# Performance work log

Measured on AMD Instinct MI355X. Metric: run time of the kernel, lower is better.

The kernel has to match this reference:

```python
import jax, jax.numpy as jnp
import numpy as np

TEMPERATURE = 1.0
MAX_ITERS = 10
EPSILON = 1e-4
N, D, K = 131072, 64, 64


def setup_inputs() -> dict:
    key = jax.random.key(0)
    k1, k2 = jax.random.split(key)
    weights = jax.random.normal(k1, (N, D), dtype=jnp.float32)
    init_clusters = jax.random.normal(k2, (K, D), dtype=jnp.float32)
    return {"weights": weights, "init_clusters": init_clusters}


def _dkm(weights, init_clusters):
    n, d = weights.shape
    k = init_clusters.shape[0]
    w_sq = jnp.sum(weights * weights, axis=1, keepdims=True)  # [N,1]

    def step(carry, _):
        clusters, attn_prev, done = carry
        # Euclidean cdist via the expansion ||w||^2 + ||c||^2 - 2 w.c
        c_sq = jnp.sum(clusters * clusters, axis=1)               # [K]
        d2 = w_sq + c_sq[None, :] - 2.0 * (weights @ clusters.T)  # [N,K]
        dist = jnp.sqrt(jnp.maximum(d2, 0.0))
        attn = jax.nn.softmax(-dist / TEMPERATURE, axis=-1)        # [N,K]
        new_clusters = (attn.T @ weights) / jnp.sum(attn, axis=0)[:, None]  # [K,D]
        converged = jnp.linalg.norm(clusters - new_clusters) <= EPSILON
        # Torch breaks BEFORE assigning new_clusters; emulate with a done flag.
        clusters_next = jnp.where(done | converged, clusters, new_clusters)
        attn_next = jnp.where(done, attn_prev, attn)
        return (clusters_next, attn_next, done | converged), None

    init = (init_clusters, jnp.zeros((n, k), weights.dtype), jnp.array(False))
    (clusters, attn, _), _ = jax.lax.scan(step, init, None, length=MAX_ITERS)
    compressed = attn @ clusters  # [N,D]
    return compressed, clusters, attn


def reference(weights, init_clusters):
    return _dkm(weights, init_clusters)
```

## Files before the change

kernel.cpp:

```cpp
#include <hip/hip_runtime.h>
#include <math.h>
#include <stdint.h>

#define N_ROWS 131072
#define DIM 64
#define KC 64
#define NBLK 512
#define ROWS_PB 256

typedef __attribute__((ext_vector_type(8))) short short8;
typedef __attribute__((ext_vector_type(8))) unsigned short ushort8;
typedef __attribute__((ext_vector_type(16))) float float16;
typedef __attribute__((ext_vector_type(4))) unsigned int uint4v;
typedef __attribute__((ext_vector_type(2))) unsigned long long ulong2v;

#define PARTIAL_OFF 0u
#define SUMA_OFF    2097152u
#define NEWC_OFF    2129920u
#define NORM_BYTE_OFF (2134016ull * 4ull)

__device__ __forceinline__ uint32_t rne16(float a) {
  uint32_t u = __float_as_uint(a);
  return (u + 0x7fffu + ((u >> 16) & 1u)) >> 16;
}

__device__ __forceinline__ uint32_t pack_bf16(float a, float b) {
  return rne16(a) | (rne16(b) << 16);
}

__device__ __forceinline__ void split2(float a, float b, uint32_t& hi, uint32_t& lo) {
  uint32_t ha = rne16(a), hb = rne16(b);
  hi = ha | (hb << 16);
  float la = a - __uint_as_float(ha << 16);
  float lb = b - __uint_as_float(hb << 16);
  lo = pack_bf16(la, lb);
}

__global__ __launch_bounds__(256, 3) void dkm_iter(
    const float* __restrict__ W, const float* __restrict__ Cinit,
    const float* __restrict__ newC, float* __restrict__ cur,
    const double* __restrict__ normpart,
    float* __restrict__ partial, float* __restrict__ sumA,
    float* __restrict__ attn_out, int useSel, int writeAttn)
{
  __shared__ __align__(16) short CbfHi[64][68];
  __shared__ __align__(16) short CbfLo[64][68];
  __shared__ __align__(16) short attnT[64][136];
  __shared__ __align__(16) short WTsh[64][136];
  __shared__ float csqL[64];
  __shared__ float wsqL[128];
  __shared__ int s_cond;

  const int t = threadIdx.x;
  const int blk = blockIdx.x;
  const int wid = t >> 6, lane = t & 63, l31 = lane & 31, lh = lane >> 5;
  const int mg = wid >> 1, ng = wid & 1;
  const int rowBase = blk * ROWS_PB;
  const int colA = wid * 32 + l31;

  const float* pwBase = W + (size_t)(rowBase + wid * 32 + l31) * 64 + lh * 8;
  float4 vv[8];
#pragma unroll
  for (int q = 0; q < 8; ++q)
    vv[q] = *(const float4*)(pwBase + (q >> 1) * 16 + (q & 1) * 4);

  if (wid == 0) {
    double v = 0.0;
    if (useSel) {
#pragma unroll
      for (int i = 0; i < 8; ++i) v += normpart[lane + 64 * i];
    }
    v += __shfl_xor(v, 1); v += __shfl_xor(v, 2); v += __shfl_xor(v, 4);
    v += __shfl_xor(v, 8); v += __shfl_xor(v, 16); v += __shfl_xor(v, 32);
    if (lane == 0) s_cond = (v > 1.0e-8) ? 1 : 0;
  }
  __syncthreads();

  const float* src = useSel ? (s_cond ? newC : cur) : Cinit;

  {
    const int crow = t >> 2, cc = (t & 3) * 16;
    float sq = 0.f;
#pragma unroll
    for (int q = 0; q < 4; ++q) {
      float4 c0 = *(const float4*)(src + crow * 64 + cc + q * 4);
      if (blk == 0) *(float4*)(cur + crow * 64 + cc + q * 4) = c0;
      uint32_t h0, h1, l0, l1;
      split2(c0.x, c0.y, h0, l0);
      split2(c0.z, c0.w, h1, l1);
      uint32_t* ph = (uint32_t*)&CbfHi[crow][cc + q * 4];
      ph[0] = h0; ph[1] = h1;
      uint32_t* pl = (uint32_t*)&CbfLo[crow][cc + q * 4];
      pl[0] = l0; pl[1] = l1;
      sq += c0.x*c0.x + c0.y*c0.y + c0.z*c0.z + c0.w*c0.w;
    }
    sq += __shfl_xor(sq, 1);
    sq += __shfl_xor(sq, 2);
    if ((t & 3) == 0) csqL[crow] = sq;
  }
  __syncthreads();

  float16 Uacc = {0,0,0,0, 0,0,0,0, 0,0,0,0, 0,0,0,0};
  float ssumAll = 0.f;
  const float cq0 = csqL[l31], cq1 = csqL[32 + l31];

#pragma unroll
  for (int c = 0; c < 2; ++c) {
    const int chunkBase = rowBase + c * 128;

    float16 dot0 = {0,0,0,0, 0,0,0,0, 0,0,0,0, 0,0,0,0};
    float16 dot1 = {0,0,0,0, 0,0,0,0, 0,0,0,0, 0,0,0,0};
    float w2acc = 0.f;
#pragma unroll
    for (int ko = 0; ko < 4; ++ko) {
      float4 a = vv[ko * 2];
      float4 b = vv[ko * 2 + 1];
      w2acc += a.x*a.x + a.y*a.y + a.z*a.z + a.w*a.w
             + b.x*b.x + b.y*b.y + b.z*b.z + b.w*b.w;
      uint32_t h0, h1, h2, h3, l0, l1, l2, l3;
      split2(a.x, a.y, h0, l0); split2(a.z, a.w, h1, l1);
      split2(b.x, b.y, h2, l2); split2(b.z, b.w, h3, l3);
      const int d0 = ko * 16 + lh * 8;
      WTsh[d0 + 0][colA] = (short)h0;  WTsh[d0 + 1][colA] = (short)(h0 >> 16);
      WTsh[d0 + 2][colA] = (short)h1;  WTsh[d0 + 3][colA] = (short)(h1 >> 16);
      WTsh[d0 + 4][colA] = (short)h2;  WTsh[d0 + 5][colA] = (short)(h2 >> 16);
      WTsh[d0 + 6][colA] = (short)h3;  WTsh[d0 + 7][colA] = (short)(h3 >> 16);
      uint4v th = {h0, h1, h2, h3};
      uint4v tl = {l0, l1, l2, l3};
      short8 aHi = __builtin_bit_cast(short8, th);
      short8 aLo = __builtin_bit_cast(short8, tl);
#pragma unroll
      for (int nt = 0; nt < 2; ++nt) {
        const unsigned long long* ph = (const unsigned long long*)&CbfHi[nt * 32 + l31][ko * 16 + lh * 8];
        const unsigned long long* pl = (const unsigned long long*)&CbfLo[nt * 32 + l31][ko * 16 + lh * 8];
        ulong2v vh = {ph[0], ph[1]};
        ulong2v vl = {pl[0], pl[1]};
        short8 cHi = __builtin_bit_cast(short8, vh);
        short8 cLo = __builtin_bit_cast(short8, vl);
        float16& dd = nt ? dot1 : dot0;
        dd = __builtin_amdgcn_mfma_f32_32x32x16_bf16(aHi, cHi, dd, 0, 0, 0);
        dd = __builtin_amdgcn_mfma_f32_32x32x16_bf16(aLo, cHi, dd, 0, 0, 0);
        dd = __builtin_amdgcn_mfma_f32_32x32x16_bf16(aHi, cLo, dd, 0, 0, 0);
      }
    }
    w2acc += __shfl_xor(w2acc, 32);
    if (lane < 32) wsqL[wid * 32 + l31] = w2acc;

    if (c == 0) {
      const float* pwN = pwBase + 128 * 64;
#pragma unroll
      for (int q = 0; q < 8; ++q)
        vv[q] = *(const float4*)(pwN + (q >> 1) * 16 + (q & 1) * 4);
    }

#pragma unroll
    for (int j = 0; j < 16; ++j) {
      const int trow = (j & 3) + 8 * (j >> 2) + 4 * lh;
      const float w2 = wsqL[wid * 32 + trow];
      float g0 = -sqrtf(fmaxf(fmaf(-2.f, dot0[j], w2 + cq0), 0.f));
      float g1 = -sqrtf(fmaxf(fmaf(-2.f, dot1[j], w2 + cq1), 0.f));
      dot0[j] = __expf(g0);
      dot1[j] = __expf(g1);
    }

    if (writeAttn) {
#pragma unroll
      for (int j = 0; j < 16; ++j) {
        const int trow = (j & 3) + 8 * (j >> 2) + 4 * lh;
        float sj = dot0[j] + dot1[j];
        sj += __shfl_xor(sj, 1);  sj += __shfl_xor(sj, 2);  sj += __shfl_xor(sj, 4);
        sj += __shfl_xor(sj, 8);  sj += __shfl_xor(sj, 16);
        float inv = __builtin_amdgcn_rcpf(sj);
        attn_out[(size_t)(chunkBase + wid * 32 + trow) * 64 + l31] = dot0[j] * inv;
        attn_out[(size_t)(chunkBase + wid * 32 + trow) * 64 + 32 + l31] = dot1[j] * inv;
      }
    }

    {
      uint32_t* aT = (uint32_t*)&attnT[0][0];
      const int cb = wid * 16;
#pragma unroll
      for (int h = 0; h < 4; ++h) {
        const int base = cb + 4 * h + 2 * lh;
        aT[l31 * 68 + base]     = pack_bf16(dot0[4 * h],     dot0[4 * h + 1]);
        aT[l31 * 68 + base + 1] = pack_bf16(dot0[4 * h + 2], dot0[4 * h + 3]);
        aT[(32 + l31) * 68 + base]     = pack_bf16(dot1[4 * h],     dot1[4 * h + 1]);
        aT[(32 + l31) * 68 + base + 1] = pack_bf16(dot1[4 * h + 2], dot1[4 * h + 3]);
      }
    }
    __syncthreads();

    float* invsL = wsqL;
    {
      const int r = t >> 1, kh = t & 1;
      float s = 0.f;
#pragma unroll
      for (int kk = 0; kk < 32; ++kk) {
        uint32_t v = (uint32_t)(unsigned short)attnT[kh * 32 + kk][r];
        s += __uint_as_float(v << 16);
      }
      s += __shfl_xor(s, 1);
      if (kh == 0) invsL[r] = __builtin_amdgcn_rcpf(s);
    }
    __syncthreads();

    {
      const int k = t >> 2, q = t & 3;
      uint32_t* row = (uint32_t*)&attnT[k][0];
#pragma unroll
      for (int i = 0; i < 16; ++i) {
        const int ii = (i + k) & 15;
        const int r2 = q * 32 + 2 * ii;
        uint32_t dv = row[q * 16 + ii];
        float lo = __uint_as_float(dv << 16) * invsL[r2];
        float hi = __uint_as_float(dv & 0xffff0000u) * invsL[r2 + 1];
        row[q * 16 + ii] = pack_bf16(lo, hi);
      }
    }
    __syncthreads();

#pragma unroll
    for (int kc = 0; kc < 8; ++kc) {
      const unsigned long long* pa =
          (const unsigned long long*)&attnT[mg * 32 + l31][kc * 16 + lh * 8];
      ulong2v va = {pa[0], pa[1]};
      short8 af = __builtin_bit_cast(short8, va);
      const unsigned long long* pb =
          (const unsigned long long*)&WTsh[ng * 32 + l31][kc * 16 + lh * 8];
      ulong2v vb = {pb[0], pb[1]};
      short8 bf = __builtin_bit_cast(short8, vb);
      Uacc = __builtin_amdgcn_mfma_f32_32x32x16_bf16(af, bf, Uacc, 0, 0, 0);
    }

    {
      const int sk = t & 63, sg = t >> 6;
#pragma unroll
      for (int q2 = 0; q2 < 4; ++q2) {
        const uint32_t* pq = (const uint32_t*)&attnT[sk][sg * 32 + q2 * 8];
#pragma unroll
        for (int w = 0; w < 4; ++w) {
          uint32_t dv = pq[w];
          ssumAll += __uint_as_float(dv << 16) + __uint_as_float(dv & 0xffff0000u);
        }
      }
    }
    __syncthreads();
  }

#pragma unroll
  for (int j = 0; j < 16; ++j) {
    const int k = mg * 32 + (j & 3) + 8 * (j >> 2) + 4 * lh;
    partial[((size_t)blk * 64 + k) * 64 + ng * 32 + l31] = Uacc[j];
  }

  float* red = (float*)&CbfHi[0][0];
  red[t] = ssumAll;
  __syncthreads();
  if (t < 64) sumA[blk * 64 + t] = (red[t] + red[t + 64]) + (red[t + 128] + red[t + 192]);
}

__global__ __launch_bounds__(256) void reduce_kernel(
    const float* __restrict__ partial, const float* __restrict__ sumAp,
    const float* __restrict__ curC, float* __restrict__ newC,
    double* __restrict__ normpart) {
  const int k = blockIdx.x >> 3, oct = blockIdx.x & 7;
  const int t = threadIdx.x;
  const int d = oct * 8 + (t & 7), q = t >> 3;
  double acc = 0.0;
  for (int b = q * 16; b < q * 16 + 16; ++b)
    acc += (double)partial[((size_t)b * 64 + k) * 64 + d];
  __shared__ double sh[256];
  __shared__ double sh2[256];
  sh[t] = acc;
  sh2[t] = (double)sumAp[t * 64 + k] + (double)sumAp[(t + 256) * 64 + k];
  __syncthreads();
#pragma unroll
  for (int s = 128; s >= 8; s >>= 1) {
    if (t < s) { sh[t] += sh[t + s]; sh2[t] += sh2[t + s]; }
    __syncthreads();
  }
#pragma unroll
  for (int s = 4; s >= 1; s >>= 1) {
    if (t < s) sh2[t] += sh2[t + s];
    __syncthreads();
  }
  if (t < 8) {
    float nc = (float)(sh[t] / sh2[0]);
    newC[k * 64 + d] = nc;
    double diff = (double)curC[k * 64 + d] - (double)nc;
    sh[t] = diff * diff;
  }
  __syncthreads();
  if (t == 0) {
    double s = 0.0;
#pragma unroll
    for (int i = 0; i < 8; ++i) s += sh[i];
    normpart[blockIdx.x] = s;
  }
}

__global__ __launch_bounds__(256) void finalize_kernel(
    const double* __restrict__ np, const float* __restrict__ newC,
    const float* __restrict__ cur, float* __restrict__ clusters_out) {
  __shared__ double sh[64];
  __shared__ int sc;
  int t = threadIdx.x;
  if (t < 64) {
    double v = 0.0;
#pragma unroll
    for (int i = 0; i < 8; ++i) v += np[t + 64 * i];
    sh[t] = v;
  }
  __syncthreads();
  if (t == 0) {
    double s = 0.0;
    for (int i = 0; i < 64; ++i) s += sh[i];
    sc = (s > 1.0e-8) ? 1 : 0;
  }
  __syncthreads();
  const float* src = sc ? newC : cur;
  for (int m = t; m < 4096; m += 256) {
    float v = src[m];
    clusters_out[m] = v;
  }
}

__global__ __launch_bounds__(256) void compress_kernel(
    const float* __restrict__ attn, const float* __restrict__ Cl,
    float* __restrict__ outC) {
  __shared__ float Csh[64 * 64];
  __shared__ float Ash[64 * 64];
  float4* Csh4 = (float4*)Csh;
  float4* Ash4 = (float4*)Ash;
  const int t = threadIdx.x;
  const int blk = blockIdx.x;
  const int rowBase = blk * 256;
  const int rg = t >> 4, dg = t & 15;

  {
    const float4* gC = (const float4*)Cl;
#pragma unroll
    for (int q = 0; q < 4; ++q) {
      int m = t + 256 * q;
      Csh4[m ^ ((m >> 6) & 15)] = gC[m];
    }
  }

  for (int tile = 0; tile < 4; ++tile) {
    __syncthreads();
    {
      const float4* gA = (const float4*)(attn + (size_t)(rowBase + tile * 64) * KC);
#pragma unroll
      for (int q = 0; q < 4; ++q) {
        int m = t + 256 * q;
        Ash4[m ^ ((m >> 6) & 15)] = gA[m];
      }
    }
    __syncthreads();
    float acc[4][4] = {{0.f}};
#pragma unroll 4
    for (int c = 0; c < 16; ++c) {
      float4 av[4], cv[4];
#pragma unroll
      for (int i = 0; i < 4; ++i) av[i] = Ash4[((rg * 4 + i) * 16 + c) ^ rg];
#pragma unroll
      for (int j = 0; j < 4; ++j) cv[j] = Csh4[((c * 4 + j) * 16 + dg) ^ c];
#pragma unroll
      for (int i = 0; i < 4; ++i) {
        float a0 = fmaf(av[i].x, cv[0].x, acc[i][0]);
        a0 = fmaf(av[i].y, cv[1].x, a0);
        a0 = fmaf(av[i].z, cv[2].x, a0);
        acc[i][0] = fmaf(av[i].w, cv[3].x, a0);
        float a1 = fmaf(av[i].x, cv[0].y, acc[i][1]);
        a1 = fmaf(av[i].y, cv[1].y, a1);
        a1 = fmaf(av[i].z, cv[2].y, a1);
        acc[i][1] = fmaf(av[i].w, cv[3].y, a1);
        float a2 = fmaf(av[i].x, cv[0].z, acc[i][2]);
        a2 = fmaf(av[i].y, cv[1].z, a2);
        a2 = fmaf(av[i].z, cv[2].z, a2);
        acc[i][2] = fmaf(av[i].w, cv[3].z, a2);
        float a3 = fmaf(av[i].x, cv[0].w, acc[i][3]);
        a3 = fmaf(av[i].y, cv[1].w, a3);
        a3 = fmaf(av[i].z, cv[2].w, a3);
        acc[i][3] = fmaf(av[i].w, cv[3].w, a3);
      }
    }
    float4* gO = (float4*)(outC + (size_t)(rowBase + tile * 64) * DIM);
#pragma unroll
    for (int i = 0; i < 4; ++i)
      gO[(rg * 4 + i) * 16 + dg] = make_float4(acc[i][0], acc[i][1], acc[i][2], acc[i][3]);
  }
}

extern "C" void kernel_launch(void* const* d_in, const int* in_sizes, int n_in,
                              void* d_out, int out_size, void* d_ws, size_t ws_size,
                              hipStream_t stream) {
  (void)in_sizes; (void)n_in; (void)d_ws; (void)ws_size; (void)out_size;
  const float* W = (const float*)d_in[0];
  const float* Cinit = (const float*)d_in[1];
  float* ob = (float*)d_out;

  float* compressed = ob;
  float* clusters_out = ob + (size_t)N_ROWS * DIM;
  float* attn_out = ob + (size_t)N_ROWS * DIM + KC * DIM;

  float* partial = ob + PARTIAL_OFF;
  float* sumAp = ob + SUMA_OFF;
  float* newC = ob + NEWC_OFF;
  float* cur = clusters_out;
  double* normpart = (double*)((char*)d_out + NORM_BYTE_OFF);

  for (int it = 0; it < 10; ++it) {
    dkm_iter<<<NBLK, 256, 0, stream>>>(W, Cinit, newC, cur, normpart,
                                       partial, sumAp, attn_out,
                                       (it > 0) ? 1 : 0, (it == 9) ? 1 : 0);
    reduce_kernel<<<512, 256, 0, stream>>>(partial, sumAp, cur, newC, normpart);
  }
  finalize_kernel<<<1, 256, 0, stream>>>(normpart, newC, cur, clusters_out);
  compress_kernel<<<512, 256, 0, stream>>>(attn_out, clusters_out, compressed);
}
```

Baseline: 354.8 us.

## Precompute transposed bf16 weights once and compute attention column sums via MFMA

Adds a prep kernel that converts W to bf16 and writes it transposed into scratch space at the start of the output buffer. The per-iteration kernel then reads the B operand for the attn^T·W MFMA straight from global memory instead of building a transposed shared-memory tile. This frees LDS, so launch bounds now allow 4 blocks per CU. The per-cluster attention sums are computed by an extra MFMA against a vector of ones, replacing the LDS scan and reduction. In exchange, each of the 10 iterations does extra global reads of the transposed copy, and workspace offsets move, which relies on later kernels overwriting that scratch region.

```diff
diff --git a/kernel.cpp b/kernel.cpp
--- a/kernel.cpp
+++ b/kernel.cpp
@@ -14,10 +14,10 @@
 typedef __attribute__((ext_vector_type(4))) unsigned int uint4v;
 typedef __attribute__((ext_vector_type(2))) unsigned long long ulong2v;
 
-#define PARTIAL_OFF 0u
-#define SUMA_OFF    2097152u
-#define NEWC_OFF    2129920u
-#define NORM_BYTE_OFF (2134016ull * 4ull)
+#define PARTIAL_OFF 4194304u
+#define SUMA_OFF    6291456u
+#define NEWC_OFF    6324224u
+#define NORM_BYTE_OFF (6328320ull * 4ull)
 
 __device__ __forceinline__ uint32_t rne16(float a) {
   uint32_t u = __float_as_uint(a);
@@ -36,8 +36,34 @@
   lo = pack_bf16(la, lb);
 }
 
-__global__ __launch_bounds__(256, 3) void dkm_iter(
-    const float* __restrict__ W, const float* __restrict__ Cinit,
+__global__ __launch_bounds__(256) void prep_kernel(const float* __restrict__ W,
+                                                   unsigned short* __restrict__ WT) {
+  __shared__ unsigned short Tsh[64][256];
+  const int t = threadIdx.x;
+  const int blk = blockIdx.x;
+  const int r = blk * 256 + t;
+  const float4* p = (const float4*)(W + (size_t)r * DIM);
+#pragma unroll
+  for (int c = 0; c < 16; ++c) {
+    float4 v = p[c];
+    Tsh[c * 4 + 0][t] = (unsigned short)rne16(v.x);
+    Tsh[c * 4 + 1][t] = (unsigned short)rne16(v.y);
+    Tsh[c * 4 + 2][t] = (unsigned short)rne16(v.z);
+    Tsh[c * 4 + 3][t] = (unsigned short)rne16(v.w);
+  }
+  __syncthreads();
+#pragma unroll
+  for (int it = 0; it < 8; ++it) {
+    const int idx = it * 256 + t;
+    const int d = idx >> 5, c8 = (idx & 31) * 8;
+    ushort8 v = *(const ushort8*)&Tsh[d][c8];
+    *(ushort8*)(WT + (size_t)d * N_ROWS + blk * 256 + c8) = v;
+  }
+}
+
+__global__ __launch_bounds__(256, 4) void dkm_iter(
+    const float* __restrict__ W, const unsigned short* __restrict__ WT,
+    const float* __restrict__ Cinit,
     const float* __restrict__ newC, float* __restrict__ cur,
     const double* __restrict__ normpart,
     float* __restrict__ partial, float* __restrict__ sumA,
@@ -46,7 +72,6 @@
   __shared__ __align__(16) short CbfHi[64][68];
   __shared__ __align__(16) short CbfLo[64][68];
   __shared__ __align__(16) short attnT[64][136];
-  __shared__ __align__(16) short WTsh[64][136];
   __shared__ float csqL[64];
   __shared__ float wsqL[128];
   __shared__ int s_cond;
@@ -56,7 +81,6 @@
   const int wid = t >> 6, lane = t & 63, l31 = lane & 31, lh = lane >> 5;
   const int mg = wid >> 1, ng = wid & 1;
   const int rowBase = blk * ROWS_PB;
-  const int colA = wid * 32 + l31;
 
   const float* pwBase = W + (size_t)(rowBase + wid * 32 + l31) * 64 + lh * 8;
   float4 vv[8];
@@ -101,7 +125,9 @@
   __syncthreads();
 
   float16 Uacc = {0,0,0,0, 0,0,0,0, 0,0,0,0, 0,0,0,0};
-  float ssumAll = 0.f;
+  float16 Uacc1 = {0,0,0,0, 0,0,0,0, 0,0,0,0, 0,0,0,0};
+  const short8 ones = {0x3F80, 0x3F80, 0x3F80, 0x3F80,
+                       0x3F80, 0x3F80, 0x3F80, 0x3F80};
   const float cq0 = csqL[l31], cq1 = csqL[32 + l31];
 
 #pragma unroll
@@ -120,11 +146,6 @@
       uint32_t h0, h1, h2, h3, l0, l1, l2, l3;
       split2(a.x, a.y, h0, l0); split2(a.z, a.w, h1, l1);
       split2(b.x, b.y, h2, l2); split2(b.z, b.w, h3, l3);
-      const int d0 = ko * 16 + lh * 8;
-      WTsh[d0 + 0][colA] = (short)h0;  WTsh[d0 + 1][colA] = (short)(h0 >> 16);
-      WTsh[d0 + 2][colA] = (short)h1;  WTsh[d0 + 3][colA] = (short)(h1 >> 16);
-      WTsh[d0 + 4][colA] = (short)h2;  WTsh[d0 + 5][colA] = (short)(h2 >> 16);
-      WTsh[d0 + 6][colA] = (short)h3;  WTsh[d0 + 7][colA] = (short)(h3 >> 16);
       uint4v th = {h0, h1, h2, h3};
       uint4v tl = {l0, l1, l2, l3};
       short8 aHi = __builtin_bit_cast(short8, th);
@@ -219,30 +240,18 @@
     }
     __syncthreads();
 
+    const unsigned short* pwt =
+        WT + (size_t)(ng * 32 + l31) * N_ROWS + chunkBase + lh * 8;
 #pragma unroll
     for (int kc = 0; kc < 8; ++kc) {
       const unsigned long long* pa =
           (const unsigned long long*)&attnT[mg * 32 + l31][kc * 16 + lh * 8];
       ulong2v va = {pa[0], pa[1]};
       short8 af = __builtin_bit_cast(short8, va);
-      const unsigned long long* pb =
-          (const unsigned long long*)&WTsh[ng * 32 + l31][kc * 16 + lh * 8];
-      ulong2v vb = {pb[0], pb[1]};
-      short8 bf = __builtin_bit_cast(short8, vb);
+      ushort8 wv = *(const ushort8*)(pwt + kc * 16);
+      short8 bf = __builtin_bit_cast(short8, wv);
       Uacc = __builtin_amdgcn_mfma_f32_32x32x16_bf16(af, bf, Uacc, 0, 0, 0);
-    }
-
-    {
-      const int sk = t & 63, sg = t >> 6;
-#pragma unroll
-      for (int q2 = 0; q2 < 4; ++q2) {
-        const uint32_t* pq = (const uint32_t*)&attnT[sk][sg * 32 + q2 * 8];
-#pragma unroll
-        for (int w = 0; w < 4; ++w) {
-          uint32_t dv = pq[w];
-          ssumAll += __uint_as_float(dv << 16) + __uint_as_float(dv & 0xffff0000u);
-        }
-      }
+      Uacc1 = __builtin_amdgcn_mfma_f32_32x32x16_bf16(af, ones, Uacc1, 0, 0, 0);
     }
     __syncthreads();
   }
@@ -252,11 +261,13 @@
     const int k = mg * 32 + (j & 3) + 8 * (j >> 2) + 4 * lh;
     partial[((size_t)blk * 64 + k) * 64 + ng * 32 + l31] = Uacc[j];
   }
-
-  float* red = (float*)&CbfHi[0][0];
-  red[t] = ssumAll;
-  __syncthreads();
-  if (t < 64) sumA[blk * 64 + t] = (red[t] + red[t + 64]) + (red[t + 128] + red[t + 192]);
+  if (ng == 0 && l31 == 0) {
+#pragma unroll
+    for (int j = 0; j < 16; ++j) {
+      const int k = mg * 32 + (j & 3) + 8 * (j >> 2) + 4 * lh;
+      sumA[blk * 64 + k] = Uacc1[j];
+    }
+  }
 }
 
 __global__ __launch_bounds__(256) void reduce_kernel(
@@ -404,14 +415,17 @@
   float* clusters_out = ob + (size_t)N_ROWS * DIM;
   float* attn_out = ob + (size_t)N_ROWS * DIM + KC * DIM;
 
+  unsigned short* WT = (unsigned short*)d_out;
   float* partial = ob + PARTIAL_OFF;
   float* sumAp = ob + SUMA_OFF;
   float* newC = ob + NEWC_OFF;
   float* cur = clusters_out;
   double* normpart = (double*)((char*)d_out + NORM_BYTE_OFF);
 
+  prep_kernel<<<NBLK, 256, 0, stream>>>(W, WT);
+
   for (int it = 0; it < 10; ++it) {
-    dkm_iter<<<NBLK, 256, 0, stream>>>(W, Cinit, newC, cur, normpart,
+    dkm_iter<<<NBLK, 256, 0, stream>>>(W, WT, Cinit, newC, cur, normpart,
                                        partial, sumAp, attn_out,
                                        (it > 0) ? 1 : 0, (it == 9) ? 1 : 0);
     reduce_kernel<<<512, 256, 0, stream>>>(partial, sumAp, cur, newC, normpart);
```

New measurement: 416.3 us. 1.17x slower.

## Precompute bf16 hi/lo split of weights once and sum attention via MFMA

Applied to the files above, without the earlier changes.

Adds a prep kernel that splits the weights into bf16 hi/lo halves and computes the row squared norms once. The results go into the attn output buffer as scratch, so the ten iterations skip the per-iteration conversion and norm work. Bytes loaded per iteration stay the same (two bf16 halves equal one fp32). The per-cluster attention sums are now computed with an extra MFMA against a ones vector, which replaces the LDS scalar reduction loop and its final barrier. The risk is that the last iteration writes attn into the same buffer the weight split lives in, while other blocks may still be reading it.

```diff
diff --git a/kernel.cpp b/kernel.cpp
--- a/kernel.cpp
+++ b/kernel.cpp
@@ -11,13 +11,13 @@
 typedef __attribute__((ext_vector_type(8))) short short8;
 typedef __attribute__((ext_vector_type(8))) unsigned short ushort8;
 typedef __attribute__((ext_vector_type(16))) float float16;
-typedef __attribute__((ext_vector_type(4))) unsigned int uint4v;
 typedef __attribute__((ext_vector_type(2))) unsigned long long ulong2v;
 
 #define PARTIAL_OFF 0u
 #define SUMA_OFF    2097152u
-#define NEWC_OFF    2129920u
-#define NORM_BYTE_OFF (2134016ull * 4ull)
+#define WSQ_OFF     2129920u
+#define NEWC_OFF    2260992u
+#define NORM_BYTE_OFF (2265088ull * 4ull)
 
 __device__ __forceinline__ uint32_t rne16(float a) {
   uint32_t u = __float_as_uint(a);
@@ -36,12 +36,35 @@
   lo = pack_bf16(la, lb);
 }
 
+__global__ __launch_bounds__(256) void prep_kernel(const float* __restrict__ W,
+                                                   unsigned short* WS,
+                                                   float* __restrict__ wsq) {
+  const int t = threadIdx.x;
+  const int r = blockIdx.x * 256 + t;
+  const float4* p = (const float4*)(W + (size_t)r * DIM);
+  uint32_t* hi = (uint32_t*)(WS + (size_t)r * 128);
+  uint32_t* lo = hi + 32;
+  float s = 0.f;
+#pragma unroll
+  for (int c = 0; c < 16; ++c) {
+    float4 v = p[c];
+    s += v.x * v.x + v.y * v.y + v.z * v.z + v.w * v.w;
+    uint32_t h0, h1, l0, l1;
+    split2(v.x, v.y, h0, l0);
+    split2(v.z, v.w, h1, l1);
+    hi[c * 2] = h0; hi[c * 2 + 1] = h1;
+    lo[c * 2] = l0; lo[c * 2 + 1] = l1;
+  }
+  wsq[r] = s;
+}
+
 __global__ __launch_bounds__(256, 3) void dkm_iter(
-    const float* __restrict__ W, const float* __restrict__ Cinit,
+    const unsigned short* WS, const float* __restrict__ wsq,
+    const float* __restrict__ Cinit,
     const float* __restrict__ newC, float* __restrict__ cur,
     const double* __restrict__ normpart,
     float* __restrict__ partial, float* __restrict__ sumA,
-    float* __restrict__ attn_out, int useSel, int writeAttn)
+    float* attn_out, int useSel, int writeAttn)
 {
   __shared__ __align__(16) short CbfHi[64][68];
   __shared__ __align__(16) short CbfLo[64][68];
@@ -58,11 +81,14 @@
   const int rowBase = blk * ROWS_PB;
   const int colA = wid * 32 + l31;
 
-  const float* pwBase = W + (size_t)(rowBase + wid * 32 + l31) * 64 + lh * 8;
-  float4 vv[8];
-#pragma unroll
-  for (int q = 0; q < 8; ++q)
-    vv[q] = *(const float4*)(pwBase + (q >> 1) * 16 + (q & 1) * 4);
+  const unsigned short* pws =
+      WS + (size_t)(rowBase + wid * 32 + l31) * 128 + lh * 8;
+  ushort8 vh[4], vl[4];
+#pragma unroll
+  for (int ko = 0; ko < 4; ++ko) {
+    vh[ko] = *(const ushort8*)(pws + ko * 16);
+    vl[ko] = *(const ushort8*)(pws + 64 + ko * 16);
+  }
 
   if (wid == 0) {
     double v = 0.0;
@@ -101,56 +127,50 @@
   __syncthreads();
 
   float16 Uacc = {0,0,0,0, 0,0,0,0, 0,0,0,0, 0,0,0,0};
-  float ssumAll = 0.f;
+  float16 Uacc1 = {0,0,0,0, 0,0,0,0, 0,0,0,0, 0,0,0,0};
+  const short8 ones = {0x3F80, 0x3F80, 0x3F80, 0x3F80,
+                       0x3F80, 0x3F80, 0x3F80, 0x3F80};
   const float cq0 = csqL[l31], cq1 = csqL[32 + l31];
 
 #pragma unroll
   for (int c = 0; c < 2; ++c) {
     const int chunkBase = rowBase + c * 128;
 
+    if (t < 128) wsqL[t] = wsq[chunkBase + t];
+
     float16 dot0 = {0,0,0,0, 0,0,0,0, 0,0,0,0, 0,0,0,0};
     float16 dot1 = {0,0,0,0, 0,0,0,0, 0,0,0,0, 0,0,0,0};
-    float w2acc = 0.f;
 #pragma unroll
     for (int ko = 0; ko < 4; ++ko) {
-      float4 a = vv[ko * 2];
-      float4 b = vv[ko * 2 + 1];
-      w2acc += a.x*a.x + a.y*a.y + a.z*a.z + a.w*a.w
-             + b.x*b.x + b.y*b.y + b.z*b.z + b.w*b.w;
-      uint32_t h0, h1, h2, h3, l0, l1, l2, l3;
-      split2(a.x, a.y, h0, l0); split2(a.z, a.w, h1, l1);
-      split2(b.x, b.y, h2, l2); split2(b.z, b.w, h3, l3);
       const int d0 = ko * 16 + lh * 8;
-      WTsh[d0 + 0][colA] = (short)h0;  WTsh[d0 + 1][colA] = (short)(h0 >> 16);
-      WTsh[d0 + 2][colA] = (short)h1;  WTsh[d0 + 3][colA] = (short)(h1 >> 16);
-      WTsh[d0 + 4][colA] = (short)h2;  WTsh[d0 + 5][colA] = (short)(h2 >> 16);
-      WTsh[d0 + 6][colA] = (short)h3;  WTsh[d0 + 7][colA] = (short)(h3 >> 16);
-      uint4v th = {h0, h1, h2, h3};
-      uint4v tl = {l0, l1, l2, l3};
-      short8 aHi = __builtin_bit_cast(short8, th);
-      short8 aLo = __builtin_bit_cast(short8, tl);
+      WTsh[d0 + 0][colA] = vh[ko][0];  WTsh[d0 + 1][colA] = vh[ko][1];
+      WTsh[d0 + 2][colA] = vh[ko][2];  WTsh[d0 + 3][colA] = vh[ko][3];
+      WTsh[d0 + 4][colA] = vh[ko][4];  WTsh[d0 + 5][colA] = vh[ko][5];
+      WTsh[d0 + 6][colA] = vh[ko][6];  WTsh[d0 + 7][colA] = vh[ko][7];
+      short8 aHi = __builtin_bit_cast(short8, vh[ko]);
+      short8 aLo = __builtin_bit_cast(short8, vl[ko]);
 #pragma unroll
       for (int nt = 0; nt < 2; ++nt) {
         const unsigned long long* ph = (const unsigned long long*)&CbfHi[nt * 32 + l31][ko * 16 + lh * 8];
         const unsigned long long* pl = (const unsigned long long*)&CbfLo[nt * 32 + l31][ko * 16 + lh * 8];
-        ulong2v vh = {ph[0], ph[1]};
-        ulong2v vl = {pl[0], pl[1]};
-        short8 cHi = __builtin_bit_cast(short8, vh);
-        short8 cLo = __builtin_bit_cast(short8, vl);
+        ulong2v vhh = {ph[0], ph[1]};
+        ulong2v vll = {pl[0], pl[1]};
+        short8 cHi = __builtin_bit_cast(short8, vhh);
+        short8 cLo = __builtin_bit_cast(short8, vll);
         float16& dd = nt ? dot1 : dot0;
         dd = __builtin_amdgcn_mfma_f32_32x32x16_bf16(aHi, cHi, dd, 0, 0, 0);
         dd = __builtin_amdgcn_mfma_f32_32x32x16_bf16(aLo, cHi, dd, 0, 0, 0);
         dd = __builtin_amdgcn_mfma_f32_32x32x16_bf16(aHi, cLo, dd, 0, 0, 0);
       }
     }
-    w2acc += __shfl_xor(w2acc, 32);
-    if (lane < 32) wsqL[wid * 32 + l31] = w2acc;
 
     if (c == 0) {
-      const float* pwN = pwBase + 128 * 64;
-#pragma unroll
-      for (int q = 0; q < 8; ++q)
-        vv[q] = *(const float4*)(pwN + (q >> 1) * 16 + (q & 1) * 4);
+      const unsigned short* pwN = pws + 128 * 128;
+#pragma unroll
+      for (int ko = 0; ko < 4; ++ko) {
+        vh[ko] = *(const ushort8*)(pwN + ko * 16);
+        vl[ko] = *(const ushort8*)(pwN + 64 + ko * 16);
+      }
     }
 
 #pragma unroll
@@ -230,19 +250,7 @@
       ulong2v vb = {pb[0], pb[1]};
       short8 bf = __builtin_bit_cast(short8, vb);
       Uacc = __builtin_amdgcn_mfma_f32_32x32x16_bf16(af, bf, Uacc, 0, 0, 0);
-    }
-
-    {
-      const int sk = t & 63, sg = t >> 6;
-#pragma unroll
-      for (int q2 = 0; q2 < 4; ++q2) {
-        const uint32_t* pq = (const uint32_t*)&attnT[sk][sg * 32 + q2 * 8];
-#pragma unroll
-        for (int w = 0; w < 4; ++w) {
-          uint32_t dv = pq[w];
-          ssumAll += __uint_as_float(dv << 16) + __uint_as_float(dv & 0xffff0000u);
-        }
-      }
+      Uacc1 = __builtin_amdgcn_mfma_f32_32x32x16_bf16(af, ones, Uacc1, 0, 0, 0);
     }
     __syncthreads();
   }
@@ -252,11 +260,13 @@
     const int k = mg * 32 + (j & 3) + 8 * (j >> 2) + 4 * lh;
     partial[((size_t)blk * 64 + k) * 64 + ng * 32 + l31] = Uacc[j];
   }
-
-  float* red = (float*)&CbfHi[0][0];
-  red[t] = ssumAll;
-  __syncthreads();
-  if (t < 64) sumA[blk * 64 + t] = (red[t] + red[t + 64]) + (red[t + 128] + red[t + 192]);
+  if (ng == 0 && l31 == 0) {
+#pragma unroll
+    for (int j = 0; j < 16; ++j) {
+      const int k = mg * 32 + (j & 3) + 8 * (j >> 2) + 4 * lh;
+      sumA[blk * 64 + k] = Uacc1[j];
+    }
+  }
 }
 
 __global__ __launch_bounds__(256) void reduce_kernel(
@@ -404,14 +414,18 @@
   float* clusters_out = ob + (size_t)N_ROWS * DIM;
   float* attn_out = ob + (size_t)N_ROWS * DIM + KC * DIM;
 
+  unsigned short* WS = (unsigned short*)attn_out;
   float* partial = ob + PARTIAL_OFF;
   float* sumAp = ob + SUMA_OFF;
+  float* wsq = ob + WSQ_OFF;
   float* newC = ob + NEWC_OFF;
   float* cur = clusters_out;
   double* normpart = (double*)((char*)d_out + NORM_BYTE_OFF);
 
+  prep_kernel<<<NBLK, 256, 0, stream>>>(W, WS, wsq);
+
   for (int it = 0; it < 10; ++it) {
-    dkm_iter<<<NBLK, 256, 0, stream>>>(W, Cinit, newC, cur, normpart,
+    dkm_iter<<<NBLK, 256, 0, stream>>>(WS, wsq, Cinit, newC, cur, normpart,
                                        partial, sumAp, attn_out,
                                        (it > 0) ? 1 : 0, (it == 9) ? 1 : 0);
     reduce_kernel<<<512, 256, 0, stream>>>(partial, sumAp, cur, newC, normpart);
```

Measured after the change: 339.7 us. 4.3% less time.
